# Kernel optimization log

Measured on AMD Instinct MI355X. Metric: run time of the kernel, lower is better.

Reference implementation:

```python
import jax, jax.numpy as jnp
import numpy as np

B, L, D = 2048, 200, 128
ITEM_D, USER_D, CAT_D, DUR_D = 64, 64, 32, 16
N_USERS, N_ITEMS, N_CAT, N_DUR = 100000, 100000, 1000, 10
UDENSE, IDENSE = 25, 3
CONCAT = USER_D + ITEM_D + CAT_D + DUR_D + UDENSE + IDENSE + D  # 332
MLP1, MLP2 = 256, 128


def setup_inputs() -> dict:
    key = jax.random.key(0)
    ks = jax.random.split(key, 24)
    f = jax.random.normal
    hist_table = 0.01 * f(ks[0], (N_ITEMS + 1, D), dtype=jnp.float32)
    hist_table = hist_table.at[0].set(0.0)  # padding_idx=0
    return {
        'user_id': jax.random.randint(ks[1], (B,), 0, N_USERS, dtype=jnp.int32),
        'item_id': jax.random.randint(ks[2], (B,), 0, N_ITEMS, dtype=jnp.int32),
        'item_category': jax.random.randint(ks[3], (B,), 0, N_CAT, dtype=jnp.int32),
        'item_dur_bkt': jax.random.randint(ks[4], (B,), 0, N_DUR, dtype=jnp.int32),
        'history_seq': jax.random.randint(ks[5], (B, L), 0, N_ITEMS + 1, dtype=jnp.int32),
        'user_dense': f(ks[6], (B, UDENSE), dtype=jnp.float32),
        'item_dense': f(ks[7], (B, IDENSE), dtype=jnp.float32),
        'user_table': 0.01 * f(ks[8], (N_USERS, USER_D), dtype=jnp.float32),
        'item_table': 0.01 * f(ks[9], (N_ITEMS, ITEM_D), dtype=jnp.float32),
        'cat_table': 0.01 * f(ks[10], (N_CAT, CAT_D), dtype=jnp.float32),
        'dur_table': 0.01 * f(ks[11], (N_DUR, DUR_D), dtype=jnp.float32),
        'hist_table': hist_table,
        'target_proj_W': f(ks[12], (D, ITEM_D), dtype=jnp.float32) / np.sqrt(ITEM_D).astype(np.float32),
        'gru_Wi': f(ks[13], (3 * D, D), dtype=jnp.float32) / np.sqrt(D).astype(np.float32),
        'gru_Wh': f(ks[14], (3 * D, D), dtype=jnp.float32) / np.sqrt(D).astype(np.float32),
        'gru_bi': jnp.zeros((3 * D,), jnp.float32),
        'gru_bh': jnp.zeros((3 * D,), jnp.float32),
        'au_Wr': f(ks[15], (D, 2 * D), dtype=jnp.float32) / np.sqrt(2 * D).astype(np.float32),
        'au_br': jnp.zeros((D,), jnp.float32),
        'au_Wu': f(ks[16], (D, 2 * D), dtype=jnp.float32) / np.sqrt(2 * D).astype(np.float32),
        'au_bu': jnp.zeros((D,), jnp.float32),
        'au_Wh': f(ks[17], (D, 2 * D), dtype=jnp.float32) / np.sqrt(2 * D).astype(np.float32),
        'au_bh': jnp.zeros((D,), jnp.float32),
        'mlp_W1': f(ks[18], (MLP1, CONCAT), dtype=jnp.float32) / np.sqrt(CONCAT).astype(np.float32),
        'mlp_b1': jnp.zeros((MLP1,), jnp.float32),
        'mlp_W2': f(ks[19], (MLP2, MLP1), dtype=jnp.float32) / np.sqrt(MLP1).astype(np.float32),
        'mlp_b2': jnp.zeros((MLP2,), jnp.float32),
        'mlp_W3': f(ks[20], (1, MLP2), dtype=jnp.float32) / np.sqrt(MLP2).astype(np.float32),
        'mlp_b3': jnp.zeros((1,), jnp.float32),
    }


def _dien_fwd(user_id, item_id, item_category, item_dur_bkt, history_seq,
              user_dense, item_dense, user_table, item_table, cat_table,
              dur_table, hist_table, target_proj_W, gru_Wi, gru_Wh, gru_bi,
              gru_bh, au_Wr, au_br, au_Wu, au_bu, au_Wh, au_bh,
              mlp_W1, mlp_b1, mlp_W2, mlp_b2, mlp_W3, mlp_b3):
    mask = history_seq > 0                      # (B, L) bool, True = real item
    hist_emb = hist_table[history_seq]          # (B, L, D)

    # ---- InterestExtractor: torch nn.GRU (eval mode, dropout off) ----
    gi = jnp.einsum('bld,ed->ble', hist_emb, gru_Wi) + gru_bi  # (B, L, 3D)

    def gru_step(h, gi_t):
        gh = h @ gru_Wh.T + gru_bh
        i_r, i_z, i_n = jnp.split(gi_t, 3, axis=-1)
        h_r, h_z, h_n = jnp.split(gh, 3, axis=-1)
        r = jax.nn.sigmoid(i_r + h_r)
        z = jax.nn.sigmoid(i_z + h_z)
        n = jnp.tanh(i_n + r * h_n)
        h_new = (1.0 - z) * n + z * h
        return h_new, h_new

    h0 = jnp.zeros((hist_emb.shape[0], D), hist_emb.dtype)
    _, hs = jax.lax.scan(gru_step, h0, jnp.swapaxes(gi, 0, 1))
    h_states = jnp.swapaxes(hs, 0, 1)           # (B, L, D)

    # ---- Target-aware attention scores ----
    i_emb = item_table[item_id]                  # (B, ITEM_D)
    target = i_emb @ target_proj_W.T             # (B, D)
    scores = jnp.einsum('bld,bd->bl', h_states, target) / np.float32(np.sqrt(D))
    scores = jnp.where(mask, scores, jnp.float32(-1e9))
    attn = jax.nn.softmax(scores, axis=-1)       # (B, L)

    # ---- InterestEvolving: AUGRU scan over L timesteps ----
    def augru_step(h, inputs):
        x_t, e_t, m_t = inputs                   # (B,D), (B,), (B,)
        comb = jnp.concatenate([x_t, h], axis=-1)
        r = jax.nn.sigmoid(comb @ au_Wr.T + au_br)
        u = jax.nn.sigmoid(comb @ au_Wu.T + au_bu)
        u_prime = e_t[:, None] * u
        h_tilde = jnp.tanh(jnp.concatenate([x_t, r * h], axis=-1) @ au_Wh.T + au_bh)
        h_new = (1.0 - u_prime) * h + u_prime * h_tilde
        valid = m_t[:, None].astype(h.dtype)
        return valid * h_new + (1.0 - valid) * h, None

    xs = (jnp.swapaxes(h_states, 0, 1), attn.T, mask.T)
    evolved, _ = jax.lax.scan(augru_step, jnp.zeros_like(h0), xs)  # (B, D)

    # ---- Final MLP head ----
    x = jnp.concatenate([
        user_table[user_id], i_emb, cat_table[item_category],
        dur_table[item_dur_bkt], user_dense, item_dense, evolved], axis=-1)
    h1 = jax.nn.relu(x @ mlp_W1.T + mlp_b1)
    h2 = jax.nn.relu(h1 @ mlp_W2.T + mlp_b2)
    logit = (h2 @ mlp_W3.T + mlp_b3)[:, 0]
    return jax.nn.sigmoid(logit)                 # (B,)


def reference(user_id, item_id, item_category, item_dur_bkt, history_seq,
              user_dense, item_dense, user_table, item_table, cat_table,
              dur_table, hist_table, target_proj_W, gru_Wi, gru_Wh, gru_bi,
              gru_bh, au_Wr, au_br, au_Wu, au_bu, au_Wh, au_bh,
              mlp_W1, mlp_b1, mlp_W2, mlp_b2, mlp_W3, mlp_b3):
    return _dien_fwd(user_id, item_id, item_category, item_dur_bkt, history_seq,
                     user_dense, item_dense, user_table, item_table, cat_table,
                     dur_table, hist_table, target_proj_W, gru_Wi, gru_Wh, gru_bi,
                     gru_bh, au_Wr, au_br, au_Wu, au_bu, au_Wh, au_bh,
                     mlp_W1, mlp_b1, mlp_W2, mlp_b2, mlp_W3, mlp_b3)
```

## Files before the change

kernel.cpp:

```cpp
#include <hip/hip_runtime.h>
#include <cstdint>
#include <cstddef>

#define BB    2048
#define LL    200
#define GR    8
#define MR    8

typedef __attribute__((ext_vector_type(4))) float f32x4;
typedef __attribute__((ext_vector_type(8))) short s16x8;

__device__ __forceinline__ float fastrcp(float x) { return __builtin_amdgcn_rcpf(x); }
__device__ __forceinline__ float sigmf(float x) { return fastrcp(1.f + __expf(-x)); }
__device__ __forceinline__ float tanh2(float x) {
    return __builtin_fmaf(2.f, fastrcp(1.f + __expf(-2.f * x)), -1.f);
}
__device__ __forceinline__ float dot4(float4 a, float4 b) {
    return a.x * b.x + a.y * b.y + a.z * b.z + a.w * b.w;
}
__device__ __forceinline__ float4 ld4(const float* p) { return *(const float4*)p; }

__device__ __forceinline__ unsigned short f2bf(float f) {
    union { float f; unsigned u; } v; v.f = f;
    unsigned r = (v.u + 0x7FFFu + ((v.u >> 16) & 1u)) >> 16;
    return (unsigned short)r;
}
__device__ __forceinline__ float bf2f(unsigned short b) {
    unsigned u = ((unsigned)b) << 16;
    union { unsigned u; float f; } v; v.u = u;
    return v.f;
}
__device__ __forceinline__ s16x8 pack8g(const float* p) {
    float4 a = ld4(p), b = ld4(p + 4);
    s16x8 o;
    o[0] = (short)f2bf(a.x); o[1] = (short)f2bf(a.y);
    o[2] = (short)f2bf(a.z); o[3] = (short)f2bf(a.w);
    o[4] = (short)f2bf(b.x); o[5] = (short)f2bf(b.y);
    o[6] = (short)f2bf(b.z); o[7] = (short)f2bf(b.w);
    return o;
}
#define MFMA(a, b, c) __builtin_amdgcn_mfma_f32_16x16x32_bf16((a), (b), (c), 0, 0, 0)

#define BAR() do { \
    asm volatile("s_waitcnt lgkmcnt(0)" ::: "memory"); \
    __builtin_amdgcn_sched_barrier(0); \
    __builtin_amdgcn_s_barrier(); \
    __builtin_amdgcn_sched_barrier(0); \
} while (0)

#define RED2(A, O0, O1) { \
    float s2_ = __shfl(A[2], srcl), s3_ = __shfl(A[3], srcl); \
    O0 = hi ? s2_ : A[0]; O1 = hi ? s3_ : A[1]; \
}

__global__ __launch_bounds__(256) void cvt_hist(const float* __restrict__ src,
                                                unsigned short* __restrict__ dst, int n8) {
    int i = blockIdx.x * 256 + threadIdx.x;
    if (i < n8) *(s16x8*)(dst + (size_t)i * 8) = pack8g(src + (size_t)i * 8);
}

__global__ void transpose_kernel(const float* __restrict__ src, float* __restrict__ dst,
                                 int rows, int cols) {
    int k = blockIdx.x;
    for (int j = threadIdx.x; j < rows; j += blockDim.x)
        dst[(size_t)k * rows + j] = src[(size_t)j * cols + k];
}

__global__ __launch_bounds__(128) void target_kernel(
    const int* __restrict__ item_id, const float* __restrict__ item_table,
    const float* __restrict__ projW, float* __restrict__ target) {
    __shared__ float ie[64];
    int b = blockIdx.x, d = threadIdx.x;
    if (d < 64) ie[d] = item_table[(size_t)item_id[b] * 64 + d];
    __syncthreads();
    float acc = 0.f;
    const float* w = projW + (size_t)d * 64;
#pragma unroll
    for (int k = 0; k < 64; k += 4) acc += dot4(ld4(&ie[k]), ld4(w + k));
    target[(size_t)b * 128 + d] = acc;
}

__global__ __launch_bounds__(512, 2) void gru_v6(
    const int* __restrict__ hseq, const unsigned short* __restrict__ hist_bf,
    const float* __restrict__ Wi, const float* __restrict__ Wh,
    const float* __restrict__ bi, const float* __restrict__ bh,
    unsigned short* __restrict__ h2) {
    __shared__ alignas(16) unsigned short xf[2][2048];
    __shared__ alignas(16) unsigned short hf[2][2048];
    __shared__ int sq[GR * LL];
    const int tid = threadIdx.x;
    const int w = tid >> 6, lane = tid & 63;
    const int b0 = blockIdx.x * GR;
    const int cb = (w << 4) | (lane & 15);
    const int kc_ = cb >> 5, kq_ = (cb >> 3) & 3, jj = cb & 7;
    const int srcl = lane & 31;
    const bool hi = lane >= 32;
    const int rowb = ((lane & 31) >> 4) * 4 + (hi ? 2 : 0);
    const int fs = ((tid >> 5) * 64 + ((tid >> 3) & 3) * 16 + (tid & 7)) * 8;
    unsigned short* const h2p = h2 + (size_t)blockIdx.x * (LL * 1024);
    s16x8 wir[4], wiz[4], win[4], whr[4], whz[4], whn[4];
    {
        int c = lane & 15, kg = (lane >> 4) * 8;
#pragma unroll
        for (int kc = 0; kc < 4; ++kc) {
            int ko = kc * 32 + kg;
            wir[kc] = pack8g(Wi + (size_t)(w * 16 + c) * 128 + ko);
            wiz[kc] = pack8g(Wi + (size_t)(128 + w * 16 + c) * 128 + ko);
            win[kc] = pack8g(Wi + (size_t)(256 + w * 16 + c) * 128 + ko);
            whr[kc] = pack8g(Wh + (size_t)(w * 16 + c) * 128 + ko);
            whz[kc] = pack8g(Wh + (size_t)(128 + w * 16 + c) * 128 + ko);
            whn[kc] = pack8g(Wh + (size_t)(256 + w * 16 + c) * 128 + ko);
        }
    }
    const float b_r = bi[cb] + bh[cb];
    const float b_z = bi[128 + cb] + bh[128 + cb];
    const float bi_n = bi[256 + cb], bh_n = bh[256 + cb];
    float hold0 = 0.f, hold1 = 0.f;
    for (int i = tid; i < 2048; i += 512) {
        xf[0][i] = 0; xf[1][i] = 0; hf[0][i] = 0; hf[1][i] = 0;
    }
    for (int i = tid; i < GR * LL; i += 512)
        sq[i] = hseq[(size_t)(b0 + i / LL) * LL + i % LL];
    __syncthreads();
    s16x8 pA, pB;
    if (lane < 16) {
        unsigned o0 = (unsigned)sq[w * LL + 0] << 7;
        *(s16x8*)&xf[0][(((lane >> 2) * 64) + (lane & 3) * 16 + w) * 8] =
            *(const s16x8*)(hist_bf + o0 + lane * 8);
        unsigned o1 = (unsigned)sq[w * LL + 1] << 7;
        pA = *(const s16x8*)(hist_bf + o1 + lane * 8);
    }
    __syncthreads();

#define GSTEP(TT, RD, CUR, NXT) { \
    const int tt = (TT); \
    if (lane < 16) { \
        *(s16x8*)&xf[RD ^ 1][(((lane >> 2) * 64) + (lane & 3) * 16 + w) * 8] = CUR; \
        unsigned no = (unsigned)sq[w * LL + (tt + 2 < LL ? tt + 2 : LL - 1)] << 7; \
        NXT = *(const s16x8*)(hist_bf + no + lane * 8); \
    } \
    if (tt > 0 && tid < 128) {   \
        s16x8 hv = *(const s16x8*)&hf[RD][fs]; \
        *(s16x8*)(h2p + (unsigned)(tt - 1) * 1024 + tid * 8) = hv; \
    } \
    f32x4 ar = {0,0,0,0}, az = {0,0,0,0}, ain = {0,0,0,0}, ahn = {0,0,0,0}; \
    _Pragma("unroll") for (int kc = 0; kc < 4; ++kc) { \
        s16x8 xa = *(const s16x8*)&xf[RD][(kc * 64 + lane) * 8]; \
        s16x8 ha = *(const s16x8*)&hf[RD][(kc * 64 + lane) * 8]; \
        ar = MFMA(xa, wir[kc], ar); ar = MFMA(ha, whr[kc], ar); \
        az = MFMA(xa, wiz[kc], az); az = MFMA(ha, whz[kc], az); \
        ain = MFMA(xa, win[kc], ain); ahn = MFMA(ha, whn[kc], ahn); \
    } \
    { \
        float r0x, r1x, z0x, z1x, ni0, ni1, nh0, nh1; \
        RED2(ar, r0x, r1x); RED2(az, z0x, z1x); \
        RED2(ain, ni0, ni1); RED2(ahn, nh0, nh1); \
        float r0 = sigmf(r0x + b_r), z0 = sigmf(z0x + b_z); \
        float n0 = tanh2(ni0 + bi_n + r0 * (nh0 + bh_n)); \
        float hv0 = (1.f - z0) * n0 + z0 * hold0; hold0 = hv0; \
        hf[RD ^ 1][(kc_ * 64 + kq_ * 16 + rowb) * 8 + jj] = (short)f2bf(hv0); \
        float r1 = sigmf(r1x + b_r), z1 = sigmf(z1x + b_z); \
        float n1 = tanh2(ni1 + bi_n + r1 * (nh1 + bh_n)); \
        float hv1 = (1.f - z1) * n1 + z1 * hold1; hold1 = hv1; \
        hf[RD ^ 1][(kc_ * 64 + kq_ * 16 + rowb + 1) * 8 + jj] = (short)f2bf(hv1); \
    } \
    BAR(); \
}

    for (int t2 = 0; t2 < LL / 2; ++t2) {
        GSTEP(2 * t2,     0, pA, pB);
        GSTEP(2 * t2 + 1, 1, pB, pA);
    }
#undef GSTEP
    if (tid < 128) {
        s16x8 hv = *(const s16x8*)&hf[0][fs];
        *(s16x8*)(h2p + (unsigned)(LL - 1) * 1024 + tid * 8) = hv;
    }
}

__global__ __launch_bounds__(512) void score_softmax2(
    const unsigned short* __restrict__ h2, const float* __restrict__ target,
    const int* __restrict__ hseq, float* __restrict__ attn) {
    __shared__ float tg[8][128];
    __shared__ float sA[8][LL];
    __shared__ float sB[8][LL];
    const int tid = threadIdx.x;
    const int blk = blockIdx.x;
    const int b0 = blk * 8;
    {
        int r = tid >> 6, d2 = (tid & 63) * 2;
        tg[r][d2] = target[(size_t)(b0 + r) * 128 + d2];
        tg[r][d2 + 1] = target[(size_t)(b0 + r) * 128 + d2 + 1];
    }
    __syncthreads();
    const unsigned short* const hp = h2 + (size_t)blk * (LL * 1024);
    const int g = tid >> 7;
    const int u = tid & 127;
    const int row = u & 7;
    const int d0 = (u >> 5) * 32 + ((u >> 3) & 3) * 8;
    const int half = u >> 6;
    for (int t = g; t < LL; t += 4) {
        s16x8 hv = *(const s16x8*)(hp + (unsigned)t * 1024 + u * 8);
        float acc = 0.f;
#pragma unroll
        for (int j = 0; j < 8; ++j)
            acc = __builtin_fmaf(bf2f((unsigned short)hv[j]), tg[row][d0 + j], acc);
        acc += __shfl_xor(acc, 8);
        acc += __shfl_xor(acc, 16);
        acc += __shfl_xor(acc, 32);
        if ((u & 63) < 8) { (half ? sB : sA)[row][t] = acc; }
    }
    __syncthreads();
    const int wv = tid >> 6, lane = tid & 63;
    float v[4];
#pragma unroll
    for (int m = 0; m < 4; ++m) {
        int t = lane + 64 * m;
        if (t < LL) {
            float s = (sA[wv][t] + sB[wv][t]) * 0.08838834764831845f;
            v[m] = (hseq[(size_t)(b0 + wv) * LL + t] > 0) ? s : -1e9f;
        } else
            v[m] = -3.0e38f;
    }
    float mx = fmaxf(fmaxf(v[0], v[1]), fmaxf(v[2], v[3]));
    for (int off = 1; off < 64; off <<= 1) mx = fmaxf(mx, __shfl_xor(mx, off));
    float s = 0.f;
#pragma unroll
    for (int m = 0; m < 4; ++m) {
        int t = lane + 64 * m;
        v[m] = (t < LL) ? __expf(v[m] - mx) : 0.f;
        s += v[m];
    }
    for (int off = 1; off < 64; off <<= 1) s += __shfl_xor(s, off);
    float inv = fastrcp(s);
#pragma unroll
    for (int m = 0; m < 4; ++m) {
        int t = lane + 64 * m;
        if (t < LL) attn[(size_t)(b0 + wv) * LL + t] = v[m] * inv;
    }
}

__global__ __launch_bounds__(512, 2) void augru_v6(
    const unsigned short* __restrict__ h2, const float* __restrict__ attn,
    const int* __restrict__ hseq,
    const float* __restrict__ Wr, const float* __restrict__ Wu,
    const float* __restrict__ Wht,
    const float* __restrict__ br, const float* __restrict__ bu,
    const float* __restrict__ bh, float* __restrict__ evolved) {
    __shared__ alignas(16) unsigned short xf[2][2048];
    __shared__ alignas(16) unsigned short hf[2][2048];
    __shared__ alignas(16) unsigned short rhf[2048];
    __shared__ float attl[GR * LL];
    __shared__ float mskl[GR * LL];
    const int tid = threadIdx.x;
    const int w = tid >> 6, lane = tid & 63;
    const int b0 = blockIdx.x * GR;
    const int cb = (w << 4) | (lane & 15);
    const int kc_ = cb >> 5, kq_ = (cb >> 3) & 3, jj = cb & 7;
    const int srcl = lane & 31;
    const bool hi = lane >= 32;
    const int rowb = ((lane & 31) >> 4) * 4 + (hi ? 2 : 0);
    const int fs = ((tid >> 5) * 64 + ((tid >> 3) & 3) * 16 + (tid & 7)) * 8;
    const unsigned short* const h2p = h2 + (size_t)blockIdx.x * (LL * 1024);
    s16x8 wr_[8], wu_[8], wx_[4], wh_[4];
    {
        int c = lane & 15, kg = (lane >> 4) * 8;
        int r0 = w * 16 + c;
#pragma unroll
        for (int kc = 0; kc < 8; ++kc) {
            wr_[kc] = pack8g(Wr + (size_t)r0 * 256 + kc * 32 + kg);
            wu_[kc] = pack8g(Wu + (size_t)r0 * 256 + kc * 32 + kg);
        }
#pragma unroll
        for (int kc = 0; kc < 4; ++kc) {
            wx_[kc] = pack8g(Wht + (size_t)r0 * 256 + kc * 32 + kg);
            wh_[kc] = pack8g(Wht + (size_t)r0 * 256 + 128 + kc * 32 + kg);
        }
    }
    const float br_c = br[cb], bu_c = bu[cb], bh_c = bh[cb];
    float hold0 = 0.f, hold1 = 0.f;
    for (int i = tid; i < 2048; i += 512) {
        xf[0][i] = 0; xf[1][i] = 0; hf[0][i] = 0; hf[1][i] = 0; rhf[i] = 0;
    }
    for (int i = tid; i < GR * LL; i += 512) {
        int r = i / LL, t = i % LL;
        attl[i] = attn[(size_t)(b0 + r) * LL + t];
        mskl[i] = (hseq[(size_t)(b0 + r) * LL + t] > 0) ? 1.f : 0.f;
    }
    __syncthreads();
    s16x8 pA, pB;
    if (tid < 128) {
        *(s16x8*)&xf[0][fs] = *(const s16x8*)(h2p + tid * 8);
        pA = *(const s16x8*)(h2p + 1024 + tid * 8);
    }
    __syncthreads();

#define ASTEP(TT, RD, CUR, NXT) { \
    const int tt = (TT); \
    if (tid < 128) { \
        *(s16x8*)&xf[RD ^ 1][fs] = CUR; \
        unsigned nt = (tt + 2 < LL ? tt + 2 : LL - 1); \
        NXT = *(const s16x8*)(h2p + nt * 1024 + tid * 8); \
    } \
    f32x4 ar = {0,0,0,0}, au = {0,0,0,0}, ax = {0,0,0,0}; \
    _Pragma("unroll") for (int kc = 0; kc < 4; ++kc) { \
        s16x8 xa = *(const s16x8*)&xf[RD][(kc * 64 + lane) * 8]; \
        s16x8 ha = *(const s16x8*)&hf[RD][(kc * 64 + lane) * 8]; \
        ar = MFMA(xa, wr_[kc], ar); ar = MFMA(ha, wr_[kc + 4], ar); \
        au = MFMA(xa, wu_[kc], au); au = MFMA(ha, wu_[kc + 4], au); \
        ax = MFMA(xa, wx_[kc], ax); \
    } \
    { \
        float a0, a1; \
        RED2(ar, a0, a1); \
        float r0 = sigmf(a0 + br_c), r1 = sigmf(a1 + br_c); \
        rhf[(kc_ * 64 + kq_ * 16 + rowb) * 8 + jj] = (short)f2bf(r0 * hold0); \
        rhf[(kc_ * 64 + kq_ * 16 + rowb + 1) * 8 + jj] = (short)f2bf(r1 * hold1); \
    } \
    BAR(); \
    f32x4 ah = {0,0,0,0}; \
    _Pragma("unroll") for (int kc = 0; kc < 4; ++kc) { \
        s16x8 ra = *(const s16x8*)&rhf[(kc * 64 + lane) * 8]; \
        ah = MFMA(ra, wh_[kc], ah); \
    } \
    { \
        float u0, u1, x0, x1, g0, g1; \
        RED2(au, u0, u1); RED2(ax, x0, x1); RED2(ah, g0, g1); \
        float uu0 = sigmf(u0 + bu_c), uu1 = sigmf(u1 + bu_c); \
        float up0 = attl[rowb * LL + tt] * uu0; \
        float up1 = attl[(rowb + 1) * LL + tt] * uu1; \
        float ht0 = tanh2(x0 + g0 + bh_c), ht1 = tanh2(x1 + g1 + bh_c); \
        float hv0 = (1.f - up0) * hold0 + up0 * ht0; \
        float hv1 = (1.f - up1) * hold1 + up1 * ht1; \
        hold0 = mskl[rowb * LL + tt] > 0.5f ? hv0 : hold0; \
        hold1 = mskl[(rowb + 1) * LL + tt] > 0.5f ? hv1 : hold1; \
        hf[RD ^ 1][(kc_ * 64 + kq_ * 16 + rowb) * 8 + jj] = (short)f2bf(hold0); \
        hf[RD ^ 1][(kc_ * 64 + kq_ * 16 + rowb + 1) * 8 + jj] = (short)f2bf(hold1); \
    } \
    BAR(); \
}

    for (int t2 = 0; t2 < LL / 2; ++t2) {
        ASTEP(2 * t2,     0, pA, pB);
        ASTEP(2 * t2 + 1, 1, pB, pA);
    }
#undef ASTEP
    evolved[(size_t)(b0 + rowb) * 128 + cb] = hold0;
    evolved[(size_t)(b0 + rowb + 1) * 128 + cb] = hold1;
}

__global__ __launch_bounds__(256) void mlp_kernel(
    const int* __restrict__ user_id, const int* __restrict__ item_id,
    const int* __restrict__ item_cat, const int* __restrict__ item_dur,
    const float* __restrict__ user_dense, const float* __restrict__ item_dense,
    const float* __restrict__ user_table, const float* __restrict__ item_table,
    const float* __restrict__ cat_table, const float* __restrict__ dur_table,
    const float* __restrict__ evolved,
    const float* __restrict__ W1t, const float* __restrict__ b1,
    const float* __restrict__ W2t, const float* __restrict__ b2,
    const float* __restrict__ W3, const float* __restrict__ b3,
    float* __restrict__ out) {
    __shared__ float Xs[MR][332];
    __shared__ float h1s[MR][256];
    __shared__ float h2s[MR][128];
    __shared__ int ids[4][MR];
    const int tid = threadIdx.x;
    const int b0 = blockIdx.x * MR;
    if (tid < MR) {
        ids[0][tid] = user_id[b0 + tid];
        ids[1][tid] = item_id[b0 + tid];
        ids[2][tid] = item_cat[b0 + tid];
        ids[3][tid] = item_dur[b0 + tid];
    }
    __syncthreads();
    for (int i = tid; i < MR * 332; i += 256) {
        int r = i / 332, c = i % 332;
        int b = b0 + r;
        float v;
        if (c < 64) v = user_table[(size_t)ids[0][r] * 64 + c];
        else if (c < 128) v = item_table[(size_t)ids[1][r] * 64 + (c - 64)];
        else if (c < 160) v = cat_table[(size_t)ids[2][r] * 32 + (c - 128)];
        else if (c < 176) v = dur_table[(size_t)ids[3][r] * 16 + (c - 160)];
        else if (c < 201) v = user_dense[(size_t)b * 25 + (c - 176)];
        else if (c < 204) v = item_dense[(size_t)b * 3 + (c - 201)];
        else v = evolved[(size_t)b * 128 + (c - 204)];
        Xs[r][c] = v;
    }
    __syncthreads();
    {
        float acc[MR] = {0, 0, 0, 0, 0, 0, 0, 0};
        for (int k = 0; k < 332; ++k) {
            float ww = W1t[(size_t)k * 256 + tid];
#pragma unroll
            for (int r = 0; r < MR; ++r) acc[r] += Xs[r][k] * ww;
        }
        float bb = b1[tid];
#pragma unroll
        for (int r = 0; r < MR; ++r) h1s[r][tid] = fmaxf(acc[r] + bb, 0.f);
    }
    __syncthreads();
    if (tid < 128) {
        float acc[MR] = {0, 0, 0, 0, 0, 0, 0, 0};
        for (int k = 0; k < 256; ++k) {
            float ww = W2t[(size_t)k * 128 + tid];
#pragma unroll
            for (int r = 0; r < MR; ++r) acc[r] += h1s[r][k] * ww;
        }
        float bb = b2[tid];
#pragma unroll
        for (int r = 0; r < MR; ++r) h2s[r][tid] = fmaxf(acc[r] + bb, 0.f);
    }
    __syncthreads();
    {
        int r = tid >> 5, j = tid & 31;
        float p = 0.f;
#pragma unroll
        for (int m = 0; m < 4; ++m) p += h2s[r][j + 32 * m] * W3[j + 32 * m];
        p += __shfl_xor(p, 16);
        p += __shfl_xor(p, 8);
        p += __shfl_xor(p, 4);
        p += __shfl_xor(p, 2);
        p += __shfl_xor(p, 1);
        if (j == 0) out[b0 + r] = 1.f / (1.f + __expf(-(p + b3[0])));
    }
}

extern "C" void kernel_launch(void* const* d_in, const int* in_sizes, int n_in,
                              void* d_out, int out_size, void* d_ws, size_t ws_size,
                              hipStream_t stream) {
    const int* user_id = (const int*)d_in[0];
    const int* item_id = (const int*)d_in[1];
    const int* item_cat = (const int*)d_in[2];
    const int* item_dur = (const int*)d_in[3];
    const int* hseq = (const int*)d_in[4];
    const float* user_dense = (const float*)d_in[5];
    const float* item_dense = (const float*)d_in[6];
    const float* user_table = (const float*)d_in[7];
    const float* item_table = (const float*)d_in[8];
    const float* cat_table = (const float*)d_in[9];
    const float* dur_table = (const float*)d_in[10];
    const float* hist_table = (const float*)d_in[11];
    const float* projW = (const float*)d_in[12];
    const float* gWi = (const float*)d_in[13];
    const float* gWh = (const float*)d_in[14];
    const float* gbi = (const float*)d_in[15];
    const float* gbh = (const float*)d_in[16];
    const float* aWr = (const float*)d_in[17];
    const float* abr = (const float*)d_in[18];
    const float* aWu = (const float*)d_in[19];
    const float* abu = (const float*)d_in[20];
    const float* aWh = (const float*)d_in[21];
    const float* abh = (const float*)d_in[22];
    const float* mW1 = (const float*)d_in[23];
    const float* mb1 = (const float*)d_in[24];
    const float* mW2 = (const float*)d_in[25];
    const float* mb2 = (const float*)d_in[26];
    const float* mW3 = (const float*)d_in[27];
    const float* mb3 = (const float*)d_in[28];
    float* out = (float*)d_out;

    float* ws = (float*)d_ws;
    float* target = ws;
    unsigned short* h2 = (unsigned short*)(ws + 262144);
    float* attn = ws + 262144 + 26214400;
    float* evolved = attn + 409600;
    float* W1t = evolved + 262144;
    float* W2t = W1t + 84992;
    unsigned short* hist_bf = (unsigned short*)(W2t + 32768);

    const int n8 = 100001 * 16;
    hipLaunchKernelGGL(cvt_hist, dim3((n8 + 255) / 256), dim3(256), 0, stream,
                       hist_table, hist_bf, n8);
    hipLaunchKernelGGL(transpose_kernel, dim3(332), dim3(256), 0, stream, mW1, W1t, 256, 332);
    hipLaunchKernelGGL(transpose_kernel, dim3(256), dim3(128), 0, stream, mW2, W2t, 128, 256);
    hipLaunchKernelGGL(target_kernel, dim3(2048), dim3(128), 0, stream,
                       item_id, item_table, projW, target);
    hipLaunchKernelGGL(gru_v6, dim3(BB / GR), dim3(512), 0, stream,
                       hseq, hist_bf, gWi, gWh, gbi, gbh, h2);
    hipLaunchKernelGGL(score_softmax2, dim3(BB / 8), dim3(512), 0, stream,
                       h2, target, hseq, attn);
    hipLaunchKernelGGL(augru_v6, dim3(BB / GR), dim3(512), 0, stream,
                       h2, attn, hseq, aWr, aWu, aWh, abr, abu, abh, evolved);
    hipLaunchKernelGGL(mlp_kernel, dim3(BB / MR), dim3(256), 0, stream,
                       user_id, item_id, item_cat, item_dur, user_dense, item_dense,
                       user_table, item_table, cat_table, dur_table, evolved,
                       W1t, mb1, W2t, mb2, mW3, mb3, out);
}
```

Measured before the change: 450.5 us.

## Load GRU/AUGRU input operands directly from global into MFMA registers

Both recurrent kernels now load each step's input fragment straight from global memory into the MFMA A-operand registers, so every wave loads its own copy. This removes the shared-memory staging buffers xf and their LDS write/read traffic. The next step's input is prefetched right after the input-side MFMAs, and the hidden-side MFMAs are issued first. In the AUGRU kernel the padding mask is folded into the attention weights (zero attention leaves the state unchanged), which drops the mask array and the select. The cost is redundant global or L2 reads across the 8 waves and less latency hiding for the prefetch.

```diff
diff --git a/kernel.cpp b/kernel.cpp
--- a/kernel.cpp
+++ b/kernel.cpp
@@ -80,12 +80,11 @@
     target[(size_t)b * 128 + d] = acc;
 }
 
-__global__ __launch_bounds__(512, 2) void gru_v6(
+__global__ __launch_bounds__(512, 2) void gru_v8(
     const int* __restrict__ hseq, const unsigned short* __restrict__ hist_bf,
     const float* __restrict__ Wi, const float* __restrict__ Wh,
     const float* __restrict__ bi, const float* __restrict__ bh,
     unsigned short* __restrict__ h2) {
-    __shared__ alignas(16) unsigned short xf[2][2048];
     __shared__ alignas(16) unsigned short hf[2][2048];
     __shared__ int sq[GR * LL];
     const int tid = threadIdx.x;
@@ -97,6 +96,8 @@
     const bool hi = lane >= 32;
     const int rowb = ((lane & 31) >> 4) * 4 + (hi ? 2 : 0);
     const int fs = ((tid >> 5) * 64 + ((tid >> 3) & 3) * 16 + (tid & 7)) * 8;
+    const int xrow = lane & 7;
+    const int xko = (lane >> 4) * 8;
     unsigned short* const h2p = h2 + (size_t)blockIdx.x * (LL * 1024);
     s16x8 wir[4], wiz[4], win[4], whr[4], whz[4], whn[4];
     {
@@ -116,41 +117,36 @@
     const float b_z = bi[128 + cb] + bh[128 + cb];
     const float bi_n = bi[256 + cb], bh_n = bh[256 + cb];
     float hold0 = 0.f, hold1 = 0.f;
-    for (int i = tid; i < 2048; i += 512) {
-        xf[0][i] = 0; xf[1][i] = 0; hf[0][i] = 0; hf[1][i] = 0;
-    }
+    for (int i = tid; i < 2048; i += 512) { hf[0][i] = 0; hf[1][i] = 0; }
     for (int i = tid; i < GR * LL; i += 512)
         sq[i] = hseq[(size_t)(b0 + i / LL) * LL + i % LL];
     __syncthreads();
-    s16x8 pA, pB;
-    if (lane < 16) {
-        unsigned o0 = (unsigned)sq[w * LL + 0] << 7;
-        *(s16x8*)&xf[0][(((lane >> 2) * 64) + (lane & 3) * 16 + w) * 8] =
-            *(const s16x8*)(hist_bf + o0 + lane * 8);
-        unsigned o1 = (unsigned)sq[w * LL + 1] << 7;
-        pA = *(const s16x8*)(hist_bf + o1 + lane * 8);
-    }
-    __syncthreads();
-
-#define GSTEP(TT, RD, CUR, NXT) { \
+
+    s16x8 x0, x1, x2, x3;
+#define XLOAD(TT) { \
+    int idx_ = sq[xrow * LL + (TT)]; \
+    const unsigned short* xp_ = hist_bf + ((size_t)idx_ << 7) + xko; \
+    x0 = *(const s16x8*)(xp_);      x1 = *(const s16x8*)(xp_ + 32); \
+    x2 = *(const s16x8*)(xp_ + 64); x3 = *(const s16x8*)(xp_ + 96); \
+}
+    XLOAD(0);
+
+#define GSTEP(TT, RD) { \
     const int tt = (TT); \
-    if (lane < 16) { \
-        *(s16x8*)&xf[RD ^ 1][(((lane >> 2) * 64) + (lane & 3) * 16 + w) * 8] = CUR; \
-        unsigned no = (unsigned)sq[w * LL + (tt + 2 < LL ? tt + 2 : LL - 1)] << 7; \
-        NXT = *(const s16x8*)(hist_bf + no + lane * 8); \
-    } \
     if (tt > 0 && tid < 128) {   \
         s16x8 hv = *(const s16x8*)&hf[RD][fs]; \
         *(s16x8*)(h2p + (unsigned)(tt - 1) * 1024 + tid * 8) = hv; \
     } \
     f32x4 ar = {0,0,0,0}, az = {0,0,0,0}, ain = {0,0,0,0}, ahn = {0,0,0,0}; \
     _Pragma("unroll") for (int kc = 0; kc < 4; ++kc) { \
-        s16x8 xa = *(const s16x8*)&xf[RD][(kc * 64 + lane) * 8]; \
         s16x8 ha = *(const s16x8*)&hf[RD][(kc * 64 + lane) * 8]; \
-        ar = MFMA(xa, wir[kc], ar); ar = MFMA(ha, whr[kc], ar); \
-        az = MFMA(xa, wiz[kc], az); az = MFMA(ha, whz[kc], az); \
-        ain = MFMA(xa, win[kc], ain); ahn = MFMA(ha, whn[kc], ahn); \
-    } \
+        ar = MFMA(ha, whr[kc], ar); az = MFMA(ha, whz[kc], az); ahn = MFMA(ha, whn[kc], ahn); \
+    } \
+    ar = MFMA(x0, wir[0], ar); az = MFMA(x0, wiz[0], az); ain = MFMA(x0, win[0], ain); \
+    ar = MFMA(x1, wir[1], ar); az = MFMA(x1, wiz[1], az); ain = MFMA(x1, win[1], ain); \
+    ar = MFMA(x2, wir[2], ar); az = MFMA(x2, wiz[2], az); ain = MFMA(x2, win[2], ain); \
+    ar = MFMA(x3, wir[3], ar); az = MFMA(x3, wiz[3], az); ain = MFMA(x3, win[3], ain); \
+    XLOAD(tt + 1 < LL ? tt + 1 : LL - 1); \
     { \
         float r0x, r1x, z0x, z1x, ni0, ni1, nh0, nh1; \
         RED2(ar, r0x, r1x); RED2(az, z0x, z1x); \
@@ -168,10 +164,11 @@
 }
 
     for (int t2 = 0; t2 < LL / 2; ++t2) {
-        GSTEP(2 * t2,     0, pA, pB);
-        GSTEP(2 * t2 + 1, 1, pB, pA);
+        GSTEP(2 * t2,     0);
+        GSTEP(2 * t2 + 1, 1);
     }
 #undef GSTEP
+#undef XLOAD
     if (tid < 128) {
         s16x8 hv = *(const s16x8*)&hf[0][fs];
         *(s16x8*)(h2p + (unsigned)(LL - 1) * 1024 + tid * 8) = hv;
@@ -240,18 +237,16 @@
     }
 }
 
-__global__ __launch_bounds__(512, 2) void augru_v6(
+__global__ __launch_bounds__(512, 2) void augru_v8(
     const unsigned short* __restrict__ h2, const float* __restrict__ attn,
     const int* __restrict__ hseq,
     const float* __restrict__ Wr, const float* __restrict__ Wu,
     const float* __restrict__ Wht,
     const float* __restrict__ br, const float* __restrict__ bu,
     const float* __restrict__ bh, float* __restrict__ evolved) {
-    __shared__ alignas(16) unsigned short xf[2][2048];
     __shared__ alignas(16) unsigned short hf[2][2048];
     __shared__ alignas(16) unsigned short rhf[2048];
     __shared__ float attl[GR * LL];
-    __shared__ float mskl[GR * LL];
     const int tid = threadIdx.x;
     const int w = tid >> 6, lane = tid & 63;
     const int b0 = blockIdx.x * GR;
@@ -260,8 +255,8 @@
     const int srcl = lane & 31;
     const bool hi = lane >= 32;
     const int rowb = ((lane & 31) >> 4) * 4 + (hi ? 2 : 0);
-    const int fs = ((tid >> 5) * 64 + ((tid >> 3) & 3) * 16 + (tid & 7)) * 8;
-    const unsigned short* const h2p = h2 + (size_t)blockIdx.x * (LL * 1024);
+    const unsigned lofs = (unsigned)((lane >> 4) * 128 + (lane & 7) * 16);
+    const char* const h2c = (const char*)(h2 + (size_t)blockIdx.x * (LL * 1024));
     s16x8 wr_[8], wu_[8], wx_[4], wh_[4];
     {
         int c = lane & 15, kg = (lane >> 4) * 8;
@@ -279,37 +274,34 @@
     }
     const float br_c = br[cb], bu_c = bu[cb], bh_c = bh[cb];
     float hold0 = 0.f, hold1 = 0.f;
-    for (int i = tid; i < 2048; i += 512) {
-        xf[0][i] = 0; xf[1][i] = 0; hf[0][i] = 0; hf[1][i] = 0; rhf[i] = 0;
-    }
+    for (int i = tid; i < 2048; i += 512) { hf[0][i] = 0; hf[1][i] = 0; rhf[i] = 0; }
     for (int i = tid; i < GR * LL; i += 512) {
         int r = i / LL, t = i % LL;
-        attl[i] = attn[(size_t)(b0 + r) * LL + t];
-        mskl[i] = (hseq[(size_t)(b0 + r) * LL + t] > 0) ? 1.f : 0.f;
-    }
-    __syncthreads();
-    s16x8 pA, pB;
-    if (tid < 128) {
-        *(s16x8*)&xf[0][fs] = *(const s16x8*)(h2p + tid * 8);
-        pA = *(const s16x8*)(h2p + 1024 + tid * 8);
-    }
-    __syncthreads();
-
-#define ASTEP(TT, RD, CUR, NXT) { \
+        float a = attn[(size_t)(b0 + r) * LL + t];
+        attl[i] = (hseq[(size_t)(b0 + r) * LL + t] > 0) ? a : 0.f;
+    }
+    __syncthreads();
+
+    s16x8 x0, x1, x2, x3;
+#define XLOADA(TT) { \
+    const char* xp_ = h2c + (unsigned)(TT) * 2048 + lofs; \
+    x0 = *(const s16x8*)(xp_);        x1 = *(const s16x8*)(xp_ + 512); \
+    x2 = *(const s16x8*)(xp_ + 1024); x3 = *(const s16x8*)(xp_ + 1536); \
+}
+    XLOADA(0);
+
+#define ASTEP(TT, RD) { \
     const int tt = (TT); \
-    if (tid < 128) { \
-        *(s16x8*)&xf[RD ^ 1][fs] = CUR; \
-        unsigned nt = (tt + 2 < LL ? tt + 2 : LL - 1); \
-        NXT = *(const s16x8*)(h2p + nt * 1024 + tid * 8); \
-    } \
     f32x4 ar = {0,0,0,0}, au = {0,0,0,0}, ax = {0,0,0,0}; \
     _Pragma("unroll") for (int kc = 0; kc < 4; ++kc) { \
-        s16x8 xa = *(const s16x8*)&xf[RD][(kc * 64 + lane) * 8]; \
         s16x8 ha = *(const s16x8*)&hf[RD][(kc * 64 + lane) * 8]; \
-        ar = MFMA(xa, wr_[kc], ar); ar = MFMA(ha, wr_[kc + 4], ar); \
-        au = MFMA(xa, wu_[kc], au); au = MFMA(ha, wu_[kc + 4], au); \
-        ax = MFMA(xa, wx_[kc], ax); \
-    } \
+        ar = MFMA(ha, wr_[kc + 4], ar); au = MFMA(ha, wu_[kc + 4], au); \
+    } \
+    ar = MFMA(x0, wr_[0], ar); au = MFMA(x0, wu_[0], au); ax = MFMA(x0, wx_[0], ax); \
+    ar = MFMA(x1, wr_[1], ar); au = MFMA(x1, wu_[1], au); ax = MFMA(x1, wx_[1], ax); \
+    ar = MFMA(x2, wr_[2], ar); au = MFMA(x2, wu_[2], au); ax = MFMA(x2, wx_[2], ax); \
+    ar = MFMA(x3, wr_[3], ar); au = MFMA(x3, wu_[3], au); ax = MFMA(x3, wx_[3], ax); \
+    XLOADA(tt + 1 < LL ? tt + 1 : LL - 1); \
     { \
         float a0, a1; \
         RED2(ar, a0, a1); \
@@ -324,16 +316,14 @@
         ah = MFMA(ra, wh_[kc], ah); \
     } \
     { \
-        float u0, u1, x0, x1, g0, g1; \
-        RED2(au, u0, u1); RED2(ax, x0, x1); RED2(ah, g0, g1); \
+        float u0, u1, xx0, xx1, g0, g1; \
+        RED2(au, u0, u1); RED2(ax, xx0, xx1); RED2(ah, g0, g1); \
         float uu0 = sigmf(u0 + bu_c), uu1 = sigmf(u1 + bu_c); \
         float up0 = attl[rowb * LL + tt] * uu0; \
         float up1 = attl[(rowb + 1) * LL + tt] * uu1; \
-        float ht0 = tanh2(x0 + g0 + bh_c), ht1 = tanh2(x1 + g1 + bh_c); \
-        float hv0 = (1.f - up0) * hold0 + up0 * ht0; \
-        float hv1 = (1.f - up1) * hold1 + up1 * ht1; \
-        hold0 = mskl[rowb * LL + tt] > 0.5f ? hv0 : hold0; \
-        hold1 = mskl[(rowb + 1) * LL + tt] > 0.5f ? hv1 : hold1; \
+        float ht0 = tanh2(xx0 + g0 + bh_c), ht1 = tanh2(xx1 + g1 + bh_c); \
+        hold0 = (1.f - up0) * hold0 + up0 * ht0; \
+        hold1 = (1.f - up1) * hold1 + up1 * ht1; \
         hf[RD ^ 1][(kc_ * 64 + kq_ * 16 + rowb) * 8 + jj] = (short)f2bf(hold0); \
         hf[RD ^ 1][(kc_ * 64 + kq_ * 16 + rowb + 1) * 8 + jj] = (short)f2bf(hold1); \
     } \
@@ -341,10 +331,11 @@
 }
 
     for (int t2 = 0; t2 < LL / 2; ++t2) {
-        ASTEP(2 * t2,     0, pA, pB);
-        ASTEP(2 * t2 + 1, 1, pB, pA);
+        ASTEP(2 * t2,     0);
+        ASTEP(2 * t2 + 1, 1);
     }
 #undef ASTEP
+#undef XLOADA
     evolved[(size_t)(b0 + rowb) * 128 + cb] = hold0;
     evolved[(size_t)(b0 + rowb + 1) * 128 + cb] = hold1;
 }
@@ -475,11 +466,11 @@
     hipLaunchKernelGGL(transpose_kernel, dim3(256), dim3(128), 0, stream, mW2, W2t, 128, 256);
     hipLaunchKernelGGL(target_kernel, dim3(2048), dim3(128), 0, stream,
                        item_id, item_table, projW, target);
-    hipLaunchKernelGGL(gru_v6, dim3(BB / GR), dim3(512), 0, stream,
+    hipLaunchKernelGGL(gru_v8, dim3(BB / GR), dim3(512), 0, stream,
                        hseq, hist_bf, gWi, gWh, gbi, gbh, h2);
     hipLaunchKernelGGL(score_softmax2, dim3(BB / 8), dim3(512), 0, stream,
                        h2, target, hseq, attn);
-    hipLaunchKernelGGL(augru_v6, dim3(BB / GR), dim3(512), 0, stream,
+    hipLaunchKernelGGL(augru_v8, dim3(BB / GR), dim3(512), 0, stream,
                        h2, attn, hseq, aWr, aWu, aWh, abr, abu, abh, evolved);
     hipLaunchKernelGGL(mlp_kernel, dim3(BB / MR), dim3(256), 0, stream,
                        user_id, item_id, item_cat, item_dur, user_dense, item_dense,
```

Measured after the change: 468.7 us. +4.0%, slower.
